# Performance work log

Measured on AMD Instinct MI355X. Metric: run time of the kernel, lower is better.

The kernel has to match this reference:

```python
import jax, jax.numpy as jnp
import numpy as np
import math

D, S, B = 64, 2048, 16  # head_dim, seq_len, batch (inputs stored as [D, S, B])


def setup_inputs() -> dict:
    key = jax.random.key(0)
    kq, kk, kv = jax.random.split(key, 3)
    return {
        "Q": jax.random.normal(kq, (D, S, B), dtype=jnp.float32),
        "K": jax.random.normal(kk, (D, S, B), dtype=jnp.float32),
        "V": jax.random.normal(kv, (D, S, B), dtype=jnp.float32),
        "d_k": S,
    }


def reference(Q, K, V, d_k):
    # transpose(0, 2): [D, S, B] -> [B, S, D]
    q = jnp.transpose(Q, (2, 1, 0))
    k = jnp.transpose(K, (2, 1, 0))
    v = jnp.transpose(V, (2, 1, 0))
    # bmm(_Q, K_T) * 1/sqrt(d_k): [B, S, S]
    scores = jnp.einsum("bsd,btd->bst", q, k) * (1.0 / math.sqrt(d_k))
    # original does view(-1, d_k) + Softmax over dim=1; with d_k == last dim
    # this is a softmax over the key axis. Dropout is identity in eval mode.
    probs = jax.nn.softmax(scores, axis=-1)
    out = jnp.einsum("bst,btd->bsd", probs, v)  # [B, S, D]
    # transpose(0, 2) back: [D, S, B]
    return jnp.transpose(out, (2, 1, 0))
```

## Files before the change

kernel.cpp:

```cpp
#include <hip/hip_runtime.h>

#define D_ 64
#define S_ 2048
#define B_ 16
#define QT 64
#define KVT 128

typedef short short8 __attribute__((ext_vector_type(8)));
typedef short short4a __attribute__((ext_vector_type(4)));
typedef float floatx4 __attribute__((ext_vector_type(4)));

#define SC2 (1.4426950408889634f / 45.254833995939045f)

__device__ __forceinline__ unsigned short f2bf(float f) {
  unsigned u = __builtin_bit_cast(unsigned, f);
  u += 0x7fffu + ((u >> 16) & 1u);
  return (unsigned short)(u >> 16);
}

__global__ __launch_bounds__(256) void pack_qk(const float* __restrict__ Q,
                                               const float* __restrict__ K,
                                               unsigned short* __restrict__ Qp,
                                               unsigned short* __restrict__ Kp) {
  const float* src = blockIdx.y ? K : Q;
  unsigned short* dst = blockIdx.y ? Kp : Qp;
  const int s0 = blockIdx.x * 16;
  __shared__ __align__(16) unsigned short tile[256][72];
  const int t = threadIdx.x;
#pragma unroll
  for (int i = 0; i < 16; i++) {
    int j = i * 256 + t;
    int d = j >> 6;
    int sb4 = (j & 63) * 4;
    const float4 v = *(const float4*)(src + (size_t)d * (S_ * B_) + s0 * B_ + sb4);
    float vv[4] = {v.x, v.y, v.z, v.w};
#pragma unroll
    for (int k = 0; k < 4; k++) {
      int sb = sb4 + k;
      tile[(sb & 15) * 16 + (sb >> 4)][d] = f2bf(vv[k]);
    }
  }
  __syncthreads();
#pragma unroll
  for (int i = 0; i < 8; i++) {
    int j = i * 256 + t;
    int r = j >> 3;
    int c = j & 7;
    int b = r >> 4, si = r & 15;
    uint4 v = *(const uint4*)(&tile[r][c * 8]);
    *(uint4*)(dst + ((size_t)(b * S_ + s0 + si) * D_ + c * 8)) = v;
  }
}

__global__ __launch_bounds__(256) void pack_v(const float* __restrict__ V,
                                              unsigned short* __restrict__ Vt) {
  const int s0 = blockIdx.x * 64;
  const int d0 = blockIdx.y * 16;
  __shared__ __align__(16) unsigned short tile[256][72];
  const int t = threadIdx.x;
#pragma unroll
  for (int i = 0; i < 16; i++) {
    int j = i * 256 + t;
    int dd = j >> 8;
    int sb4 = (j & 255) * 4;
    const float4 v = *(const float4*)(V + (size_t)(d0 + dd) * (S_ * B_) + s0 * B_ + sb4);
    float vv[4] = {v.x, v.y, v.z, v.w};
#pragma unroll
    for (int k = 0; k < 4; k++) {
      int sb = sb4 + k;
      tile[(sb & 15) * 16 + dd][sb >> 4] = f2bf(vv[k]);
    }
  }
  __syncthreads();
#pragma unroll
  for (int i = 0; i < 8; i++) {
    int j = i * 256 + t;
    int r = j >> 3;
    int c = j & 7;
    int b = r >> 4, dd = r & 15;
    uint4 v = *(const uint4*)(&tile[r][c * 8]);
    *(uint4*)(Vt + ((size_t)(b * D_ + d0 + dd) * S_ + s0 + c * 8)) = v;
  }
}

__global__ __launch_bounds__(256, 2) void attn(const unsigned short* __restrict__ Qp,
                                               const unsigned short* __restrict__ Kp,
                                               const unsigned short* __restrict__ Vt,
                                               float* __restrict__ Ot) {
  __shared__ __align__(16) unsigned short Qs[64 * 72];
  __shared__ __align__(16) unsigned short Ks[128 * 72];
  __shared__ __align__(16) unsigned short Vs[64 * 136];
  __shared__ __align__(16) unsigned short Ps[64 * 136];

  const int tid = threadIdx.x;
  const int w = tid >> 6, l = tid & 63, g = l >> 4, ln = l & 15;
  const int b = blockIdx.x & 15;
  const int q0 = (int)(blockIdx.x >> 4) * QT;
  const int kvw = w * 32;

#pragma unroll
  for (int i = 0; i < 2; i++) {
    int j = i * 256 + tid;
    int r = j >> 3, c = j & 7;
    uint4 v = *(const uint4*)(Qp + ((size_t)(b * S_ + q0 + r) * D_ + c * 8));
    *(uint4*)(&Qs[r * 72 + c * 8]) = v;
  }
  __syncthreads();

  short8 qf[4][2];
#pragma unroll
  for (int nf = 0; nf < 4; nf++)
#pragma unroll
    for (int ks = 0; ks < 2; ks++)
      qf[nf][ks] = *(const short8*)(&Qs[(nf * 16 + ln) * 72 + ks * 32 + g * 8]);

  floatx4 oacc[4];
#pragma unroll
  for (int nf = 0; nf < 4; nf++) oacc[nf] = (floatx4){0.f, 0.f, 0.f, 0.f};
  float lpart[4] = {0.f, 0.f, 0.f, 0.f};

  for (int kv0 = 0; kv0 < S_; kv0 += KVT) {
#pragma unroll
    for (int i = 0; i < 4; i++) {
      int j = i * 256 + tid;
      int r = j >> 3, c = j & 7;
      uint4 v = *(const uint4*)(Kp + ((size_t)(b * S_ + kv0 + r) * D_ + c * 8));
      *(uint4*)(&Ks[r * 72 + c * 8]) = v;
    }
#pragma unroll
    for (int i = 0; i < 4; i++) {
      int j = i * 256 + tid;
      int r = j >> 4, c = j & 15;
      uint4 v = *(const uint4*)(Vt + ((size_t)(b * D_ + r) * S_ + kv0 + c * 8));
      *(uint4*)(&Vs[r * 136 + c * 8]) = v;
    }
    __syncthreads();

    floatx4 sacc[2][4];
#pragma unroll
    for (int mf = 0; mf < 2; mf++)
#pragma unroll
      for (int nf = 0; nf < 4; nf++) sacc[mf][nf] = (floatx4){0.f, 0.f, 0.f, 0.f};
#pragma unroll
    for (int ks = 0; ks < 2; ks++) {
      short8 kf[2];
#pragma unroll
      for (int mf = 0; mf < 2; mf++)
        kf[mf] = *(const short8*)(&Ks[(kvw + mf * 16 + ln) * 72 + ks * 32 + g * 8]);
#pragma unroll
      for (int mf = 0; mf < 2; mf++)
#pragma unroll
        for (int nf = 0; nf < 4; nf++)
          sacc[mf][nf] = __builtin_amdgcn_mfma_f32_16x16x32_bf16(kf[mf], qf[nf][ks],
                                                                 sacc[mf][nf], 0, 0, 0);
    }

#pragma unroll
    for (int mf = 0; mf < 2; mf++)
#pragma unroll
      for (int nf = 0; nf < 4; nf++) {
        float p0 = __builtin_amdgcn_exp2f(sacc[mf][nf][0] * SC2);
        float p1 = __builtin_amdgcn_exp2f(sacc[mf][nf][1] * SC2);
        float p2 = __builtin_amdgcn_exp2f(sacc[mf][nf][2] * SC2);
        float p3 = __builtin_amdgcn_exp2f(sacc[mf][nf][3] * SC2);
        lpart[nf] += (p0 + p1) + (p2 + p3);
        short4a pk;
        pk[0] = (short)f2bf(p0); pk[1] = (short)f2bf(p1);
        pk[2] = (short)f2bf(p2); pk[3] = (short)f2bf(p3);
        *(short4a*)(&Ps[(nf * 16 + ln) * 136 + kvw + mf * 16 + g * 4]) = pk;
      }
    __syncthreads();

    short8 vf[4];
#pragma unroll
    for (int ks4 = 0; ks4 < 4; ks4++)
      vf[ks4] = *(const short8*)(&Vs[(w * 16 + ln) * 136 + ks4 * 32 + g * 8]);
#pragma unroll
    for (int nf = 0; nf < 4; nf++) {
#pragma unroll
      for (int ks4 = 0; ks4 < 4; ks4++) {
        short8 pf = *(const short8*)(&Ps[(nf * 16 + ln) * 136 + ks4 * 32 + g * 8]);
        oacc[nf] = __builtin_amdgcn_mfma_f32_16x16x32_bf16(vf[ks4], pf, oacc[nf], 0, 0, 0);
      }
    }
    __syncthreads();
  }

  float* lred = (float*)&Ps[0];
  float lsum[4];
#pragma unroll
  for (int nf = 0; nf < 4; nf++) {
    float v = lpart[nf];
    v += __shfl_xor(v, 16);
    v += __shfl_xor(v, 32);
    lsum[nf] = v;
  }
  if (g == 0) {
#pragma unroll
    for (int nf = 0; nf < 4; nf++) lred[w * 64 + nf * 16 + ln] = lsum[nf];
  }
  __syncthreads();
  float linv[4];
#pragma unroll
  for (int nf = 0; nf < 4; nf++) {
    int q = nf * 16 + ln;
    linv[nf] = 1.0f / (lred[0 * 64 + q] + lred[1 * 64 + q] + lred[2 * 64 + q] + lred[3 * 64 + q]);
  }

#pragma unroll
  for (int nf = 0; nf < 4; nf++) {
    int q = nf * 16 + ln;
#pragma unroll
    for (int r = 0; r < 4; r++) {
      int d = w * 16 + g * 4 + r;
      Ot[(size_t)(b * D_ + d) * S_ + q0 + q] = oacc[nf][r] * linv[nf];
    }
  }
}

__global__ __launch_bounds__(256) void unpack_o(const float* __restrict__ Ot,
                                                float* __restrict__ out) {
  const int d0 = (int)(blockIdx.x & 7) * 8;
  const int s0 = (int)(blockIdx.x >> 3) * 64;
  __shared__ float u[8 * 1024];
  const int t = threadIdx.x;
#pragma unroll
  for (int i = 0; i < 8; i++) {
    int j = i * 256 + t;
    int d = j >> 8, bb = (j >> 4) & 15, c = j & 15;
    float4 v = *(const float4*)(Ot + (size_t)(bb * D_ + d0 + d) * S_ + s0 + c * 4);
    float vv[4] = {v.x, v.y, v.z, v.w};
#pragma unroll
    for (int k = 0; k < 4; k++) {
      int si = c * 4 + k;
      int W = si * 16 + bb;
      int Wp = W ^ ((si & 15) << 2);
      u[d * 1024 + Wp] = vv[k];
    }
  }
  __syncthreads();
#pragma unroll
  for (int i = 0; i < 8; i++) {
    int j = i * 256 + t;
    int d = j >> 8, c2 = j & 255;
    int G = c2 ^ ((c2 >> 2) & 15);
    float4 v = *(const float4*)(&u[d * 1024 + G * 4]);
    *(float4*)(out + (size_t)(d0 + d) * (S_ * B_) + s0 * B_ + c2 * 4) = v;
  }
}

extern "C" void kernel_launch(void* const* d_in, const int* in_sizes, int n_in,
                              void* d_out, int out_size, void* d_ws, size_t ws_size,
                              hipStream_t stream) {
  const float* Q = (const float*)d_in[0];
  const float* K = (const float*)d_in[1];
  const float* V = (const float*)d_in[2];
  float* out = (float*)d_out;
  char* ws = (char*)d_ws;
  unsigned short* Qp = (unsigned short*)(ws);
  unsigned short* Kp = (unsigned short*)(ws + (4u << 20));
  unsigned short* Vt = (unsigned short*)(ws + (8u << 20));
  float* Ot = (float*)(ws + (12u << 20));

  hipLaunchKernelGGL(pack_qk, dim3(128, 2), dim3(256), 0, stream, Q, K, Qp, Kp);
  hipLaunchKernelGGL(pack_v, dim3(32, 4), dim3(256), 0, stream, V, Vt);
  hipLaunchKernelGGL(attn, dim3(512), dim3(256), 0, stream, Qp, Kp, Vt, Ot);
  hipLaunchKernelGGL(unpack_o, dim3(256), dim3(256), 0, stream, Ot, out);
}
```

Measured before the change: 115.7 us.

## Keep P in registers, prefetch K/V, fold scale into K, merge pack kernels

Merges the Q/K and V packing kernels into one launch and folds the softmax scale into K during packing. The attention kernel now loads Q and K fragments straight from global memory into registers and keeps P in registers as MFMA operands instead of staging it through shared memory. V is double-buffered in LDS with a register prefetch, and the row sums come from an MFMA against a ones vector. Each wave accumulates a partial output over its own KV slice, so a cross-wave reduction through LDS is needed at the end. The aim is fewer barriers and less LDS traffic per KV tile, at the cost of many more accumulator registers and more LDS for the final reduction, which could lower occupancy.

New measurement: 110.8 us. 4.3% less time.

```diff
diff --git a/kernel.cpp b/kernel.cpp
--- a/kernel.cpp
+++ b/kernel.cpp
@@ -9,6 +9,7 @@
 typedef short short8 __attribute__((ext_vector_type(8)));
 typedef short short4a __attribute__((ext_vector_type(4)));
 typedef float floatx4 __attribute__((ext_vector_type(4)));
+typedef unsigned uint2v __attribute__((ext_vector_type(2)));
 
 #define SC2 (1.4426950408889634f / 45.254833995939045f)
 
@@ -18,68 +19,80 @@
   return (unsigned short)(u >> 16);
 }
 
-__global__ __launch_bounds__(256) void pack_qk(const float* __restrict__ Q,
-                                               const float* __restrict__ K,
-                                               unsigned short* __restrict__ Qp,
-                                               unsigned short* __restrict__ Kp) {
-  const float* src = blockIdx.y ? K : Q;
-  unsigned short* dst = blockIdx.y ? Kp : Qp;
-  const int s0 = blockIdx.x * 16;
+__device__ __forceinline__ floatx4 mfma16(short4a a, short4a b, floatx4 c) {
+#if __has_builtin(__builtin_amdgcn_mfma_f32_16x16x16bf16_1k)
+  return __builtin_amdgcn_mfma_f32_16x16x16bf16_1k(a, b, c, 0, 0, 0);
+#else
+  floatx4 d;
+  asm volatile("v_mfma_f32_16x16x16_bf16 %0, %1, %2, %3"
+               : "=v"(d) : "v"(a), "v"(b), "v"(c));
+  return d;
+#endif
+}
+
+__global__ __launch_bounds__(256) void pack_all(const float* __restrict__ Q,
+                                                const float* __restrict__ K,
+                                                const float* __restrict__ V,
+                                                unsigned short* __restrict__ Qp,
+                                                unsigned short* __restrict__ Kp,
+                                                unsigned short* __restrict__ Vt) {
   __shared__ __align__(16) unsigned short tile[256][72];
   const int t = threadIdx.x;
-#pragma unroll
-  for (int i = 0; i < 16; i++) {
-    int j = i * 256 + t;
-    int d = j >> 6;
-    int sb4 = (j & 63) * 4;
-    const float4 v = *(const float4*)(src + (size_t)d * (S_ * B_) + s0 * B_ + sb4);
-    float vv[4] = {v.x, v.y, v.z, v.w};
-#pragma unroll
-    for (int k = 0; k < 4; k++) {
-      int sb = sb4 + k;
-      tile[(sb & 15) * 16 + (sb >> 4)][d] = f2bf(vv[k]);
-    }
-  }
-  __syncthreads();
-#pragma unroll
-  for (int i = 0; i < 8; i++) {
-    int j = i * 256 + t;
-    int r = j >> 3;
-    int c = j & 7;
-    int b = r >> 4, si = r & 15;
-    uint4 v = *(const uint4*)(&tile[r][c * 8]);
-    *(uint4*)(dst + ((size_t)(b * S_ + s0 + si) * D_ + c * 8)) = v;
-  }
-}
-
-__global__ __launch_bounds__(256) void pack_v(const float* __restrict__ V,
-                                              unsigned short* __restrict__ Vt) {
-  const int s0 = blockIdx.x * 64;
-  const int d0 = blockIdx.y * 16;
-  __shared__ __align__(16) unsigned short tile[256][72];
-  const int t = threadIdx.x;
-#pragma unroll
-  for (int i = 0; i < 16; i++) {
-    int j = i * 256 + t;
-    int dd = j >> 8;
-    int sb4 = (j & 255) * 4;
-    const float4 v = *(const float4*)(V + (size_t)(d0 + dd) * (S_ * B_) + s0 * B_ + sb4);
-    float vv[4] = {v.x, v.y, v.z, v.w};
-#pragma unroll
-    for (int k = 0; k < 4; k++) {
-      int sb = sb4 + k;
-      tile[(sb & 15) * 16 + dd][sb >> 4] = f2bf(vv[k]);
-    }
-  }
-  __syncthreads();
-#pragma unroll
-  for (int i = 0; i < 8; i++) {
-    int j = i * 256 + t;
-    int r = j >> 3;
-    int c = j & 7;
-    int b = r >> 4, dd = r & 15;
-    uint4 v = *(const uint4*)(&tile[r][c * 8]);
-    *(uint4*)(Vt + ((size_t)(b * D_ + d0 + dd) * S_ + s0 + c * 8)) = v;
+  const int bid = blockIdx.x;
+  if (bid < 256) {
+    const bool isK = bid >= 128;
+    const float* src = isK ? K : Q;
+    unsigned short* dst = isK ? Kp : Qp;
+    const float scale = isK ? SC2 : 1.0f;
+    const int s0 = (bid & 127) * 16;
+#pragma unroll
+    for (int i = 0; i < 16; i++) {
+      int j = i * 256 + t;
+      int d = j >> 6;
+      int sb4 = (j & 63) * 4;
+      const float4 v = *(const float4*)(src + (size_t)d * (S_ * B_) + s0 * B_ + sb4);
+      float vv[4] = {v.x, v.y, v.z, v.w};
+#pragma unroll
+      for (int k = 0; k < 4; k++) {
+        int sb = sb4 + k;
+        tile[(sb & 15) * 16 + (sb >> 4)][d] = f2bf(vv[k] * scale);
+      }
+    }
+    __syncthreads();
+#pragma unroll
+    for (int i = 0; i < 8; i++) {
+      int j = i * 256 + t;
+      int r = j >> 3, c = j & 7;
+      int b = r >> 4, si = r & 15;
+      uint4 v = *(const uint4*)(&tile[r][c * 8]);
+      *(uint4*)(dst + ((size_t)(b * S_ + s0 + si) * D_ + c * 8)) = v;
+    }
+  } else {
+    const int vb = bid - 256;
+    const int s0 = (vb & 31) * 64;
+    const int d0 = (vb >> 5) * 16;
+#pragma unroll
+    for (int i = 0; i < 16; i++) {
+      int j = i * 256 + t;
+      int dd = j >> 8;
+      int sb4 = (j & 255) * 4;
+      const float4 v = *(const float4*)(V + (size_t)(d0 + dd) * (S_ * B_) + s0 * B_ + sb4);
+      float vv[4] = {v.x, v.y, v.z, v.w};
+#pragma unroll
+      for (int k = 0; k < 4; k++) {
+        int sb = sb4 + k;
+        tile[(sb & 15) * 16 + dd][sb >> 4] = f2bf(vv[k]);
+      }
+    }
+    __syncthreads();
+#pragma unroll
+    for (int i = 0; i < 8; i++) {
+      int j = i * 256 + t;
+      int r = j >> 3, c = j & 7;
+      int b = r >> 4, dd = r & 15;
+      uint4 v = *(const uint4*)(&tile[r][c * 8]);
+      *(uint4*)(Vt + ((size_t)(b * D_ + d0 + dd) * S_ + s0 + c * 8)) = v;
+    }
   }
 }
 
@@ -87,10 +100,11 @@
                                                const unsigned short* __restrict__ Kp,
                                                const unsigned short* __restrict__ Vt,
                                                float* __restrict__ Ot) {
-  __shared__ __align__(16) unsigned short Qs[64 * 72];
-  __shared__ __align__(16) unsigned short Ks[128 * 72];
-  __shared__ __align__(16) unsigned short Vs[64 * 136];
-  __shared__ __align__(16) unsigned short Ps[64 * 136];
+  __shared__ __align__(16) char smem_[69632 + 1024];
+  float* red = (float*)smem_;
+  float* lred = (float*)(smem_ + 69632);
+  unsigned short* Vbuf0 = (unsigned short*)smem_;
+  unsigned short* Vbuf1 = (unsigned short*)(smem_ + 17408);
 
   const int tid = threadIdx.x;
   const int w = tid >> 6, l = tid & 63, g = l >> 4, ln = l & 15;
@@ -98,123 +112,143 @@
   const int q0 = (int)(blockIdx.x >> 4) * QT;
   const int kvw = w * 32;
 
-#pragma unroll
-  for (int i = 0; i < 2; i++) {
-    int j = i * 256 + tid;
-    int r = j >> 3, c = j & 7;
-    uint4 v = *(const uint4*)(Qp + ((size_t)(b * S_ + q0 + r) * D_ + c * 8));
-    *(uint4*)(&Qs[r * 72 + c * 8]) = v;
+  const unsigned short* Qb = Qp + (size_t)b * S_ * D_;
+  const unsigned short* Kb = Kp + (size_t)b * S_ * D_;
+  const unsigned short* Vb = Vt + (size_t)b * D_ * S_;
+
+  short8 qf[4][2];
+#pragma unroll
+  for (int nf = 0; nf < 4; nf++)
+#pragma unroll
+    for (int ks = 0; ks < 2; ks++)
+      qf[nf][ks] = *(const short8*)(Qb + (size_t)(q0 + nf * 16 + ln) * D_ + ks * 32 + g * 8);
+
+  short8 kf[2][2];
+#pragma unroll
+  for (int mf = 0; mf < 2; mf++)
+#pragma unroll
+    for (int ks = 0; ks < 2; ks++)
+      kf[mf][ks] = *(const short8*)(Kb + (size_t)(kvw + mf * 16 + ln) * D_ + ks * 32 + g * 8);
+
+  {
+    uint4 vstg[4];
+#pragma unroll
+    for (int i = 0; i < 4; i++) {
+      int idx = i * 256 + tid, r = idx >> 4, c = idx & 15;
+      vstg[i] = *(const uint4*)(Vb + (size_t)r * S_ + c * 8);
+    }
+#pragma unroll
+    for (int i = 0; i < 4; i++) {
+      int idx = i * 256 + tid, r = idx >> 4, c = idx & 15;
+      *(uint4*)(&Vbuf0[r * 136 + c * 8]) = vstg[i];
+    }
   }
   __syncthreads();
 
-  short8 qf[4][2];
-#pragma unroll
-  for (int nf = 0; nf < 4; nf++)
+  const short4a ones = {(short)0x3F80, (short)0x3F80, (short)0x3F80, (short)0x3F80};
+  floatx4 oacc[4][4];
+  floatx4 dacc[4];
+#pragma unroll
+  for (int mfd = 0; mfd < 4; mfd++)
+#pragma unroll
+    for (int nf = 0; nf < 4; nf++) oacc[mfd][nf] = (floatx4){0.f, 0.f, 0.f, 0.f};
+#pragma unroll
+  for (int nf = 0; nf < 4; nf++) dacc[nf] = (floatx4){0.f, 0.f, 0.f, 0.f};
+
+  for (int t = 0; t < 16; t++) {
+    const int kvn = ((t + 1) * KVT) & (S_ - 1);
+
+    uint4 vstg[4];
+#pragma unroll
+    for (int i = 0; i < 4; i++) {
+      int idx = i * 256 + tid, r = idx >> 4, c = idx & 15;
+      vstg[i] = *(const uint4*)(Vb + (size_t)r * S_ + kvn + c * 8);
+    }
+
+    floatx4 sacc[2][4];
+#pragma unroll
+    for (int mf = 0; mf < 2; mf++)
+#pragma unroll
+      for (int nf = 0; nf < 4; nf++) sacc[mf][nf] = (floatx4){0.f, 0.f, 0.f, 0.f};
 #pragma unroll
     for (int ks = 0; ks < 2; ks++)
-      qf[nf][ks] = *(const short8*)(&Qs[(nf * 16 + ln) * 72 + ks * 32 + g * 8]);
-
-  floatx4 oacc[4];
-#pragma unroll
-  for (int nf = 0; nf < 4; nf++) oacc[nf] = (floatx4){0.f, 0.f, 0.f, 0.f};
-  float lpart[4] = {0.f, 0.f, 0.f, 0.f};
-
-  for (int kv0 = 0; kv0 < S_; kv0 += KVT) {
+#pragma unroll
+      for (int mf = 0; mf < 2; mf++)
+#pragma unroll
+        for (int nf = 0; nf < 4; nf++)
+          sacc[mf][nf] = __builtin_amdgcn_mfma_f32_16x16x32_bf16(kf[mf][ks], qf[nf][ks],
+                                                                 sacc[mf][nf], 0, 0, 0);
+
+#pragma unroll
+    for (int mf = 0; mf < 2; mf++)
+#pragma unroll
+      for (int ks = 0; ks < 2; ks++)
+        kf[mf][ks] = *(const short8*)(Kb + (size_t)(kvn + kvw + mf * 16 + ln) * D_ + ks * 32 + g * 8);
+
+    short4a pb[2][4];
+#pragma unroll
+    for (int mf = 0; mf < 2; mf++)
+#pragma unroll
+      for (int nf = 0; nf < 4; nf++) {
+        unsigned u0 = __builtin_bit_cast(unsigned, __builtin_amdgcn_exp2f(sacc[mf][nf][0])) + 0x8000u;
+        unsigned u1 = __builtin_bit_cast(unsigned, __builtin_amdgcn_exp2f(sacc[mf][nf][1])) + 0x8000u;
+        unsigned u2 = __builtin_bit_cast(unsigned, __builtin_amdgcn_exp2f(sacc[mf][nf][2])) + 0x8000u;
+        unsigned u3 = __builtin_bit_cast(unsigned, __builtin_amdgcn_exp2f(sacc[mf][nf][3])) + 0x8000u;
+        unsigned lo = __builtin_amdgcn_perm(u1, u0, 0x07060302u);
+        unsigned hi = __builtin_amdgcn_perm(u3, u2, 0x07060302u);
+        pb[mf][nf] = __builtin_bit_cast(short4a, (uint2v){lo, hi});
+      }
+
+#pragma unroll
+    for (int mf = 0; mf < 2; mf++)
+#pragma unroll
+      for (int nf = 0; nf < 4; nf++)
+        dacc[nf] = mfma16(ones, pb[mf][nf], dacc[nf]);
+
+    unsigned short* vw = ((t + 1) & 1) ? Vbuf1 : Vbuf0;
 #pragma unroll
     for (int i = 0; i < 4; i++) {
-      int j = i * 256 + tid;
-      int r = j >> 3, c = j & 7;
-      uint4 v = *(const uint4*)(Kp + ((size_t)(b * S_ + kv0 + r) * D_ + c * 8));
-      *(uint4*)(&Ks[r * 72 + c * 8]) = v;
-    }
-#pragma unroll
-    for (int i = 0; i < 4; i++) {
-      int j = i * 256 + tid;
-      int r = j >> 4, c = j & 15;
-      uint4 v = *(const uint4*)(Vt + ((size_t)(b * D_ + r) * S_ + kv0 + c * 8));
-      *(uint4*)(&Vs[r * 136 + c * 8]) = v;
-    }
-    __syncthreads();
-
-    floatx4 sacc[2][4];
-#pragma unroll
-    for (int mf = 0; mf < 2; mf++)
-#pragma unroll
-      for (int nf = 0; nf < 4; nf++) sacc[mf][nf] = (floatx4){0.f, 0.f, 0.f, 0.f};
-#pragma unroll
-    for (int ks = 0; ks < 2; ks++) {
-      short8 kf[2];
-#pragma unroll
-      for (int mf = 0; mf < 2; mf++)
-        kf[mf] = *(const short8*)(&Ks[(kvw + mf * 16 + ln) * 72 + ks * 32 + g * 8]);
-#pragma unroll
-      for (int mf = 0; mf < 2; mf++)
+      int idx = i * 256 + tid, r = idx >> 4, c = idx & 15;
+      *(uint4*)(&vw[r * 136 + c * 8]) = vstg[i];
+    }
+
+    const unsigned short* vr = (t & 1) ? Vbuf1 : Vbuf0;
+#pragma unroll
+    for (int mfd = 0; mfd < 4; mfd++)
+#pragma unroll
+      for (int mf = 0; mf < 2; mf++) {
+        short4a vf = *(const short4a*)(&vr[(mfd * 16 + ln) * 136 + kvw + mf * 16 + g * 4]);
 #pragma unroll
         for (int nf = 0; nf < 4; nf++)
-          sacc[mf][nf] = __builtin_amdgcn_mfma_f32_16x16x32_bf16(kf[mf], qf[nf][ks],
-                                                                 sacc[mf][nf], 0, 0, 0);
-    }
-
-#pragma unroll
-    for (int mf = 0; mf < 2; mf++)
-#pragma unroll
-      for (int nf = 0; nf < 4; nf++) {
-        float p0 = __builtin_amdgcn_exp2f(sacc[mf][nf][0] * SC2);
-        float p1 = __builtin_amdgcn_exp2f(sacc[mf][nf][1] * SC2);
-        float p2 = __builtin_amdgcn_exp2f(sacc[mf][nf][2] * SC2);
-        float p3 = __builtin_amdgcn_exp2f(sacc[mf][nf][3] * SC2);
-        lpart[nf] += (p0 + p1) + (p2 + p3);
-        short4a pk;
-        pk[0] = (short)f2bf(p0); pk[1] = (short)f2bf(p1);
-        pk[2] = (short)f2bf(p2); pk[3] = (short)f2bf(p3);
-        *(short4a*)(&Ps[(nf * 16 + ln) * 136 + kvw + mf * 16 + g * 4]) = pk;
+          oacc[mfd][nf] = mfma16(vf, pb[mf][nf], oacc[mfd][nf]);
       }
     __syncthreads();
-
-    short8 vf[4];
-#pragma unroll
-    for (int ks4 = 0; ks4 < 4; ks4++)
-      vf[ks4] = *(const short8*)(&Vs[(w * 16 + ln) * 136 + ks4 * 32 + g * 8]);
-#pragma unroll
-    for (int nf = 0; nf < 4; nf++) {
-#pragma unroll
-      for (int ks4 = 0; ks4 < 4; ks4++) {
-        short8 pf = *(const short8*)(&Ps[(nf * 16 + ln) * 136 + ks4 * 32 + g * 8]);
-        oacc[nf] = __builtin_amdgcn_mfma_f32_16x16x32_bf16(vf[ks4], pf, oacc[nf], 0, 0, 0);
-      }
-    }
-    __syncthreads();
-  }
-
-  float* lred = (float*)&Ps[0];
-  float lsum[4];
-#pragma unroll
-  for (int nf = 0; nf < 4; nf++) {
-    float v = lpart[nf];
-    v += __shfl_xor(v, 16);
-    v += __shfl_xor(v, 32);
-    lsum[nf] = v;
-  }
+  }
+
   if (g == 0) {
 #pragma unroll
-    for (int nf = 0; nf < 4; nf++) lred[w * 64 + nf * 16 + ln] = lsum[nf];
-  }
+    for (int nf = 0; nf < 4; nf++) lred[w * 64 + nf * 16 + ln] = dacc[nf][0];
+  }
+#pragma unroll
+  for (int mfd = 0; mfd < 4; mfd++)
+#pragma unroll
+    for (int nf = 0; nf < 4; nf++)
+      *(floatx4*)(&red[w * 4352 + (nf * 16 + ln) * 68 + mfd * 16 + g * 4]) = oacc[mfd][nf];
   __syncthreads();
-  float linv[4];
-#pragma unroll
-  for (int nf = 0; nf < 4; nf++) {
-    int q = nf * 16 + ln;
-    linv[nf] = 1.0f / (lred[0 * 64 + q] + lred[1 * 64 + q] + lred[2 * 64 + q] + lred[3 * 64 + q]);
-  }
-
-#pragma unroll
-  for (int nf = 0; nf < 4; nf++) {
-    int q = nf * 16 + ln;
-#pragma unroll
-    for (int r = 0; r < 4; r++) {
-      int d = w * 16 + g * 4 + r;
-      Ot[(size_t)(b * D_ + d) * S_ + q0 + q] = oacc[nf][r] * linv[nf];
-    }
+
+  const int q = l;
+  const float denom = lred[q] + lred[64 + q] + lred[128 + q] + lred[192 + q];
+  const float linv = 1.0f / denom;
+#pragma unroll
+  for (int i = 0; i < 4; i++) {
+    floatx4 s = (floatx4){0.f, 0.f, 0.f, 0.f};
+#pragma unroll
+    for (int w2 = 0; w2 < 4; w2++)
+      s += *(const floatx4*)(&red[w2 * 4352 + q * 68 + w * 16 + i * 4]);
+    s *= linv;
+#pragma unroll
+    for (int r = 0; r < 4; r++)
+      Ot[(size_t)(b * D_ + w * 16 + i * 4 + r) * S_ + q0 + q] = s[r];
   }
 }
 
@@ -262,8 +296,7 @@
   unsigned short* Vt = (unsigned short*)(ws + (8u << 20));
   float* Ot = (float*)(ws + (12u << 20));
 
-  hipLaunchKernelGGL(pack_qk, dim3(128, 2), dim3(256), 0, stream, Q, K, Qp, Kp);
-  hipLaunchKernelGGL(pack_v, dim3(32, 4), dim3(256), 0, stream, V, Vt);
+  hipLaunchKernelGGL(pack_all, dim3(384), dim3(256), 0, stream, Q, K, V, Qp, Kp, Vt);
   hipLaunchKernelGGL(attn, dim3(512), dim3(256), 0, stream, Qp, Kp, Vt, Ot);
   hipLaunchKernelGGL(unpack_o, dim3(256), dim3(256), 0, stream, Ot, out);
 }
```
